# Optimization experiments

Measured on AMD Instinct MI355X. Metric: run time of the kernel, lower is better.

## Reference

```python
import jax, jax.numpy as jnp
import numpy as np

D_MODEL = 2048
N_HEADS = 16
HEAD_DIM = D_MODEL // N_HEADS
THETA = 10000.0


def setup_inputs() -> dict:
    key = jax.random.key(0)
    k1, k2, k3 = jax.random.split(key, 3)
    B, S = 4, 2048
    x = jax.random.normal(k1, (B, S, D_MODEL), dtype=jnp.float32)
    std_qkv = (2.0 / (D_MODEL + 3 * D_MODEL)) ** 0.5
    w_qkv = jax.random.normal(k2, (3 * D_MODEL, D_MODEL), dtype=jnp.float32) * std_qkv
    std_o = (2.0 / (D_MODEL + D_MODEL)) ** 0.5
    w_out = jax.random.normal(k3, (D_MODEL, D_MODEL), dtype=jnp.float32) * std_o
    return {"x": x, "w_qkv": w_qkv, "w_out": w_out}


def _rope(t, cos, sin):
    # t: [H, B, S, hd]; cos/sin: [S, hd/2]; interleaved (even/odd) pairs
    t1 = t[..., 0::2]
    t2 = t[..., 1::2]
    r1 = t1 * cos - t2 * sin
    r2 = t1 * sin + t2 * cos
    return jnp.stack([r1, r2], axis=-1).reshape(t.shape)


def reference(x, w_qkv, w_out):
    B, S, _ = x.shape
    qkv = jnp.einsum('bsd,od->bso', x, w_qkv)  # [B,S,3*D]
    qkv = qkv.reshape(B, S, 3, N_HEADS, HEAD_DIM).transpose(2, 3, 0, 1, 4)  # [3,H,B,S,hd]
    q, k, v = qkv[0], qkv[1], qkv[2]

    pos = jnp.arange(S, dtype=jnp.float32)
    inv_freq = THETA ** (-(jnp.arange(0, HEAD_DIM, 2, dtype=jnp.float32) / HEAD_DIM))
    freqs = pos[:, None] * inv_freq[None, :]  # [S, hd/2]
    cos, sin = jnp.cos(freqs), jnp.sin(freqs)
    q = _rope(q, cos, sin)
    k = _rope(k, cos, sin)

    scores = jnp.einsum('hbqd,hbkd->hbqk', q, k) / jnp.sqrt(jnp.float32(HEAD_DIM))
    causal = jnp.tril(jnp.ones((S, S), dtype=bool))
    scores = jnp.where(causal, scores, -jnp.inf)
    p = jax.nn.softmax(scores, axis=-1)
    a = jnp.einsum('hbqk,hbkd->hbqd', p, v)  # [H,B,S,hd]
    a = a.transpose(1, 2, 0, 3).reshape(B, S, N_HEADS * HEAD_DIM)
    return jnp.einsum('bsd,od->bso', a, w_out)
```

## Files before the change

### kernel.cpp

```cpp
#include <hip/hip_runtime.h>
#include <hip/hip_bf16.h>

typedef __attribute__((ext_vector_type(8))) __bf16 bf16x8;
typedef __attribute__((ext_vector_type(4))) __bf16 bf16x4;
typedef __attribute__((ext_vector_type(4))) float f32x4;
typedef __attribute__((ext_vector_type(4))) unsigned int uintx4;
typedef __attribute__((ext_vector_type(2))) unsigned int uintx2;

__device__ __forceinline__ unsigned short f2bf(float f) {
  __bf16 h = (__bf16)f;
  return __builtin_bit_cast(unsigned short, h);
}
__device__ __forceinline__ float bf2f(unsigned short u) {
  unsigned int x = ((unsigned int)u) << 16;
  return __builtin_bit_cast(float, x);
}
__device__ __forceinline__ bf16x8 ld_frag(const unsigned short* p) {
  return __builtin_bit_cast(bf16x8, *reinterpret_cast<const uintx4*>(p));
}
__device__ __forceinline__ uintx2 cvt4(float4 v) {
  bf16x4 h = { (__bf16)v.x, (__bf16)v.y, (__bf16)v.z, (__bf16)v.w };
  return __builtin_bit_cast(uintx2, h);
}
__device__ __forceinline__ void gload16(const unsigned short* g, unsigned short* l) {
  __builtin_amdgcn_global_load_lds(
      (const __attribute__((address_space(1))) void*)g,
      (__attribute__((address_space(3))) void*)l, 16, 0, 0);
}

__device__ __forceinline__ void cvt8(const float* in, unsigned short* out, int gid) {
  const float4* p = reinterpret_cast<const float4*>(in) + (size_t)gid * 2;
  float4 a = p[0], b = p[1];
  uintx2 lo = cvt4(a), hi = cvt4(b);
  uintx4 o = { lo[0], lo[1], hi[0], hi[1] };
  *(reinterpret_cast<uintx4*>(out) + gid) = o;
}

__global__ __launch_bounds__(256)
void prep(const float* __restrict__ x, unsigned short* __restrict__ xb,
          const float* __restrict__ wqkv, unsigned short* __restrict__ wqkvb,
          float2* __restrict__ tab) {
  const int bid = blockIdx.x, tid = threadIdx.x;
  if (bid < 8192) {
    cvt8(x, xb, bid * 256 + tid);
  } else if (bid < 14336) {
    cvt8(wqkv, wqkvb, (bid - 8192) * 256 + tid);
  } else {
    int gid = (bid - 14336) * 256 + tid;
    int i = gid & 63, s = gid >> 6;
    double inv = pow(10000.0, -(double)i / 64.0);
    double ang = (double)s * inv;
    tab[gid] = make_float2((float)cos(ang), (float)sin(ang));
  }
}

__global__ __launch_bounds__(256)
void cvt_bf16(const float* __restrict__ in, unsigned short* __restrict__ out, int n8) {
  int gid = blockIdx.x * 256 + threadIdx.x;
  if (gid >= n8) return;
  cvt8(in, out, gid);
}

__global__ __launch_bounds__(256)
void rope_kernel(unsigned short* __restrict__ qb, unsigned short* __restrict__ kb,
                 const float2* __restrict__ tab) {
  int gid = blockIdx.x * 256 + threadIdx.x;
  int g = gid & 15;
  int s = (gid >> 4) & 2047;
  int hb = (gid >> 15) & 63;
  unsigned short* base = (gid >> 21) ? kb : qb;
  size_t off = (((size_t)hb * 2048 + s) * 128) + g * 8;
  union { uintx4 u; unsigned short sh[8]; } v;
  v.u = *reinterpret_cast<const uintx4*>(base + off);
  #pragma unroll
  for (int p = 0; p < 4; ++p) {
    float2 cs = tab[s * 64 + g * 4 + p];
    float x1 = bf2f(v.sh[2 * p]), x2 = bf2f(v.sh[2 * p + 1]);
    float r1 = x1 * cs.x - x2 * cs.y;
    float r2 = x1 * cs.y + x2 * cs.x;
    v.sh[2 * p] = f2bf(r1);
    v.sh[2 * p + 1] = f2bf(r2);
  }
  *reinterpret_cast<uintx4*>(base + off) = v.u;
}

template<int EPI>
__global__ __launch_bounds__(512, 1)
void gemm8(const unsigned short* __restrict__ A, const unsigned short* __restrict__ B,
           float* __restrict__ C, unsigned short* __restrict__ qb,
           unsigned short* __restrict__ kb, unsigned short* __restrict__ vtb,
           int M, int N, int K, int nbx) {
  __shared__ unsigned short Al[2][256 * 64];
  __shared__ unsigned short Bl[2][256 * 64];
  const int nwg = gridDim.x, bid = blockIdx.x;
  const int swz = (bid & 7) * (nwg >> 3) + (bid >> 3);
  const int n0 = (swz % nbx) * 256, m0 = (swz / nbx) * 256;
  const int tid = threadIdx.x, lane = tid & 63, w = tid >> 6;
  const int wr = w >> 2, wc = w & 3, l15 = lane & 15, l4 = lane >> 4;
  const int NT = K >> 6;

  auto stage_half = [&](const unsigned short* src, int gr0, unsigned short* ldsb, int kt) {
    #pragma unroll
    for (int i = 0; i < 2; ++i) {
      const int rb = (w * 2 + i) * 8;
      const int R = rb + (lane >> 3);
      const int cs = ((lane & 7) * 8) ^ ((R & 7) << 3);
      gload16(&src[(size_t)(gr0 + R) * K + kt + cs], &ldsb[rb * 64]);
    }
  };
  auto sp_a0b0 = [&](int J) {
    const int buf = J & 1, kt = J * 64;
    stage_half(A, m0, &Al[buf][0], kt);
    stage_half(B, n0, &Bl[buf][0], kt);
  };
  auto sp_b1a1 = [&](int J) {
    const int buf = J & 1, kt = J * 64;
    stage_half(B, n0 + 128, &Bl[buf][128 * 64], kt);
    stage_half(A, m0 + 128, &Al[buf][128 * 64], kt);
  };

  f32x4 acc[8][4];
  const f32x4 z = {0.f, 0.f, 0.f, 0.f};
  #pragma unroll
  for (int mi = 0; mi < 8; ++mi)
    #pragma unroll
    for (int ni = 0; ni < 4; ++ni) acc[mi][ni] = z;

  bf16x8 aF[4][2], bF[4][2];
  auto ldA = [&](int buf, int mh) {
    #pragma unroll
    for (int i = 0; i < 4; ++i) {
      const int R = wr * 128 + (mh * 4 + i) * 16 + l15;
      #pragma unroll
      for (int kk = 0; kk < 2; ++kk)
        aF[i][kk] = ld_frag(&Al[buf][R * 64 + ((kk * 32 + l4 * 8) ^ ((R & 7) << 3))]);
    }
  };
  auto ldB = [&](int buf, int nh) {
    #pragma unroll
    for (int i = 0; i < 2; ++i) {
      const int R = wc * 64 + (nh * 2 + i) * 16 + l15;
      #pragma unroll
      for (int kk = 0; kk < 2; ++kk)
        bF[nh * 2 + i][kk] = ld_frag(&Bl[buf][R * 64 + ((kk * 32 + l4 * 8) ^ ((R & 7) << 3))]);
    }
  };
  auto mm = [&](int mh, int nh) {
    __builtin_amdgcn_s_setprio(1);
    #pragma unroll
    for (int i = 0; i < 4; ++i)
      #pragma unroll
      for (int ii = 0; ii < 2; ++ii)
        #pragma unroll
        for (int kk = 0; kk < 2; ++kk)
          acc[mh * 4 + i][nh * 2 + ii] = __builtin_amdgcn_mfma_f32_16x16x32_bf16(
              aF[i][kk], bF[nh * 2 + ii][kk], acc[mh * 4 + i][nh * 2 + ii], 0, 0, 0);
    __builtin_amdgcn_s_setprio(0);
  };

  sp_a0b0(0); sp_b1a1(0); sp_a0b0(1);
  asm volatile("s_waitcnt vmcnt(4)" ::: "memory");
  __builtin_amdgcn_s_barrier();

  for (int J = 0; J < NT; ++J) {
    const int buf = J & 1;
    ldA(buf, 0);
    ldB(buf, 0);
    if (J + 1 < NT) sp_b1a1(J + 1);
    __builtin_amdgcn_s_barrier();
    asm volatile("s_waitcnt lgkmcnt(0)" ::: "memory");
    mm(0, 0);
    __builtin_amdgcn_s_barrier();
    ldB(buf, 1);
    __builtin_amdgcn_s_barrier();
    asm volatile("s_waitcnt lgkmcnt(0)" ::: "memory");
    mm(0, 1);
    __builtin_amdgcn_s_barrier();
    ldA(buf, 1);
    __builtin_amdgcn_s_barrier();
    asm volatile("s_waitcnt lgkmcnt(0)" ::: "memory");
    mm(1, 0);
    __builtin_amdgcn_s_barrier();
    if (J + 2 < NT) sp_a0b0(J + 2);
    asm volatile("s_waitcnt vmcnt(4)" ::: "memory");
    __builtin_amdgcn_s_barrier();
    mm(1, 1);
    __builtin_amdgcn_s_barrier();
  }

  if constexpr (EPI == 0) {
    #pragma unroll
    for (int mi = 0; mi < 8; ++mi)
      #pragma unroll
      for (int ni = 0; ni < 4; ++ni) {
        const int col = n0 + wc * 64 + ni * 16 + l15;
        #pragma unroll
        for (int j = 0; j < 4; ++j) {
          const int row = m0 + wr * 128 + mi * 16 + l4 * 4 + j;
          C[(size_t)row * N + col] = acc[mi][ni][j];
        }
      }
  } else {
    #pragma unroll
    for (int ni = 0; ni < 4; ++ni) {
      const int col = n0 + wc * 64 + ni * 16 + l15;
      const int t = col >> 11, h = (col >> 7) & 15, d = col & 127;
      #pragma unroll
      for (int mi = 0; mi < 8; ++mi) {
        const int row0 = m0 + wr * 128 + mi * 16 + l4 * 4;
        const int b = row0 >> 11, s0 = row0 & 2047;
        if (t == 2) {
          bf16x4 v4 = { (__bf16)acc[mi][ni][0], (__bf16)acc[mi][ni][1],
                        (__bf16)acc[mi][ni][2], (__bf16)acc[mi][ni][3] };
          *reinterpret_cast<uintx2*>(&vtb[(((size_t)(h * 4 + b)) * 128 + d) * 2048 + s0]) =
              __builtin_bit_cast(uintx2, v4);
        } else {
          unsigned short* base = t ? kb : qb;
          #pragma unroll
          for (int j = 0; j < 4; ++j)
            base[(((size_t)(h * 4 + b)) * 2048 + s0 + j) * 128 + d] = f2bf(acc[mi][ni][j]);
        }
      }
    }
  }
}

__global__ __launch_bounds__(512)
void attn_kernel(const unsigned short* __restrict__ q,
                 const unsigned short* __restrict__ k,
                 const unsigned short* __restrict__ vt,
                 unsigned short* __restrict__ a) {
  const int hb = blockIdx.x;
  const int h = hb >> 2, b = hb & 3;
  const int Q = 15 - blockIdx.y;
  const int q0 = Q * 128;
  const int tid = threadIdx.x, w = tid >> 6, lane = tid & 63;
  const int l15 = lane & 15, l4 = lane >> 4;

  __shared__ unsigned short Klds[64 * 128];
  __shared__ unsigned short Vlds[128 * 64];
  __shared__ unsigned short Plds[8][16 * 64];

  const size_t qkbase = (size_t)hb * 2048 * 128;
  const size_t vtbase = (size_t)hb * 128 * 2048;
  const int qw_min = q0 + w * 16;
  const float scale = 0.08838834764831845f;
  const int nt = 2 * Q + 2;

  bf16x8 qf[4];
  #pragma unroll
  for (int ks = 0; ks < 4; ++ks)
    qf[ks] = ld_frag(&q[qkbase + (size_t)(qw_min + l15) * 128 + ks * 32 + l4 * 8]);

  uintx4 kreg[2], vreg[2];
  auto issue = [&](int kt) {
    #pragma unroll
    for (int i = 0; i < 2; ++i) {
      const int slot = tid + i * 512;
      kreg[i] = *reinterpret_cast<const uintx4*>(
          &k[qkbase + (size_t)(kt + (slot >> 4)) * 128 + (slot & 15) * 8]);
      vreg[i] = *reinterpret_cast<const uintx4*>(
          &vt[vtbase + (size_t)(slot >> 3) * 2048 + kt + (slot & 7) * 8]);
    }
  };
  auto commit = [&]() {
    #pragma unroll
    for (int i = 0; i < 2; ++i) {
      const int slot = tid + i * 512;
      const int kr = slot >> 4, kc = (slot & 15) * 8;
      *reinterpret_cast<uintx4*>(&Klds[kr * 128 + (kc ^ ((kr & 7) << 3))]) = kreg[i];
      const int vr = slot >> 3, vc = (slot & 7) * 8;
      *reinterpret_cast<uintx4*>(&Vlds[vr * 64 + (vc ^ ((vr & 7) << 3))]) = vreg[i];
    }
  };

  float m[4], lsum[4];
  f32x4 acco[8];
  const f32x4 z = {0.f, 0.f, 0.f, 0.f};
  #pragma unroll
  for (int j = 0; j < 4; ++j) { m[j] = -1e30f; lsum[j] = 0.f; }
  #pragma unroll
  for (int d2 = 0; d2 < 8; ++d2) acco[d2] = z;

  issue(0);
  commit();
  __syncthreads();

  for (int t = 0; t < nt; ++t) {
    const int kt = t * 64;
    if (t + 1 < nt) issue(kt + 64);

    f32x4 sc[4];
    #pragma unroll
    for (int c = 0; c < 4; ++c) sc[c] = z;
    __builtin_amdgcn_s_setprio(1);
    #pragma unroll
    for (int c = 0; c < 4; ++c) {
      const int kr = c * 16 + l15;
      #pragma unroll
      for (int ks = 0; ks < 4; ++ks) {
        bf16x8 kf = ld_frag(&Klds[kr * 128 + ((l4 * 8 + ks * 32) ^ ((kr & 7) << 3))]);
        sc[c] = __builtin_amdgcn_mfma_f32_16x16x32_bf16(qf[ks], kf, sc[c], 0, 0, 0);
      }
    }
    __builtin_amdgcn_s_setprio(0);

    #pragma unroll
    for (int c = 0; c < 4; ++c) {
      const int kvg = kt + c * 16 + l15;
      #pragma unroll
      for (int j = 0; j < 4; ++j) {
        const int qg = qw_min + l4 * 4 + j;
        float s = sc[c][j] * scale;
        sc[c][j] = (kvg > qg) ? -1e30f : s;
      }
    }
    float mx[4];
    #pragma unroll
    for (int j = 0; j < 4; ++j)
      mx[j] = fmaxf(fmaxf(sc[0][j], sc[1][j]), fmaxf(sc[2][j], sc[3][j]));
    #pragma unroll
    for (int off = 1; off < 16; off <<= 1)
      #pragma unroll
      for (int j = 0; j < 4; ++j) mx[j] = fmaxf(mx[j], __shfl_xor(mx[j], off));
    bool need = false;
    #pragma unroll
    for (int j = 0; j < 4; ++j) need |= (mx[j] > m[j] + 8.0f);
    if (__any(need)) {
      #pragma unroll
      for (int j = 0; j < 4; ++j) {
        float nm = fmaxf(m[j], mx[j]);
        float al = __expf(m[j] - nm);
        m[j] = nm;
        lsum[j] *= al;
        #pragma unroll
        for (int d2 = 0; d2 < 8; ++d2) acco[d2][j] *= al;
      }
    }
    float rs[4] = {0.f, 0.f, 0.f, 0.f};
    #pragma unroll
    for (int c = 0; c < 4; ++c)
      #pragma unroll
      for (int j = 0; j < 4; ++j) {
        float p = __expf(sc[c][j] - m[j]);
        sc[c][j] = p;
        rs[j] += p;
      }
    #pragma unroll
    for (int off = 1; off < 16; off <<= 1)
      #pragma unroll
      for (int j = 0; j < 4; ++j) rs[j] += __shfl_xor(rs[j], off);
    #pragma unroll
    for (int j = 0; j < 4; ++j) lsum[j] += rs[j];

    #pragma unroll
    for (int c = 0; c < 4; ++c)
      #pragma unroll
      for (int j = 0; j < 4; ++j) {
        const int qr = l4 * 4 + j;
        const int kv = c * 16 + l15;
        Plds[w][qr * 64 + (kv ^ ((qr & 7) << 3))] = f2bf(sc[c][j]);
      }
    __builtin_amdgcn_s_setprio(1);
    #pragma unroll
    for (int g = 0; g < 2; ++g) {
      bf16x8 pf = ld_frag(&Plds[w][l15 * 64 + ((g * 32 + l4 * 8) ^ ((l15 & 7) << 3))]);
      #pragma unroll
      for (int d2 = 0; d2 < 8; ++d2) {
        const int dr = d2 * 16 + l15;
        bf16x8 vf = ld_frag(&Vlds[dr * 64 + ((g * 32 + l4 * 8) ^ ((dr & 7) << 3))]);
        acco[d2] = __builtin_amdgcn_mfma_f32_16x16x32_bf16(pf, vf, acco[d2], 0, 0, 0);
      }
    }
    __builtin_amdgcn_s_setprio(0);

    __syncthreads();
    if (t + 1 < nt) {
      commit();
      __syncthreads();
    }
  }

  #pragma unroll
  for (int j = 0; j < 4; ++j) {
    const float inv = 1.0f / lsum[j];
    const int sr = qw_min + l4 * 4 + j;
    const size_t abase = ((size_t)(b * 2048 + sr)) * 2048 + h * 128;
    #pragma unroll
    for (int d2 = 0; d2 < 8; ++d2)
      a[abase + d2 * 16 + l15] = f2bf(acco[d2][j] * inv);
  }
}

extern "C" void kernel_launch(void* const* d_in, const int* in_sizes, int n_in,
                              void* d_out, int out_size, void* d_ws, size_t ws_size,
                              hipStream_t stream) {
  const float* x = (const float*)d_in[0];
  const float* wqkv = (const float*)d_in[1];
  const float* wout = (const float*)d_in[2];
  float* out = (float*)d_out;
  char* ws = (char*)d_ws;
  char* ob = (char*)d_out;

  unsigned short* qbuf = (unsigned short*)(ws + 0);
  unsigned short* kbuf = (unsigned short*)(ws + 33554432);
  unsigned short* vtb  = (unsigned short*)(ws + 67108864);
  unsigned short* abuf = (unsigned short*)(ws + 100663296);
  unsigned short* woutb = qbuf;
  unsigned short* xb    = (unsigned short*)(ob + 0);
  unsigned short* wqkvb = (unsigned short*)(ob + 33554432);
  float2*         tab   = (float2*)(ob + 58720256);

  hipLaunchKernelGGL(prep, dim3(14848), dim3(256), 0, stream,
                     x, xb, wqkv, wqkvb, tab);
  hipLaunchKernelGGL((gemm8<1>), dim3(768), dim3(512), 0, stream,
                     xb, wqkvb, nullptr, qbuf, kbuf, vtb, 8192, 6144, 2048, 24);
  hipLaunchKernelGGL(rope_kernel, dim3(16384), dim3(256), 0, stream,
                     qbuf, kbuf, (const float2*)tab);
  hipLaunchKernelGGL(attn_kernel, dim3(64, 16), dim3(512), 0, stream,
                     qbuf, kbuf, vtb, abuf);
  hipLaunchKernelGGL(cvt_bf16, dim3(2048), dim3(256), 0, stream, wout, woutb, 524288);
  hipLaunchKernelGGL((gemm8<0>), dim3(256), dim3(512), 0, stream,
                     abuf, woutb, out, nullptr, nullptr, nullptr, 8192, 2048, 2048, 8);
}
```

Before: 497.4 us.

## Fuse RoPE into QKV GEMM epilogue and restructure GEMM LDS pipeline

Removes the standalone RoPE kernel and applies the rotation inside the QKV GEMM epilogue, using a lane shuffle to fetch each pair partner. This drops one full read/write pass over the Q and K buffers. The GEMM main loop is also reorganised: fragments are split into separate A0/A1/B0/B1 registers, and the next tile's first fragments are prefetched before the loop iteration ends. Global staging is regrouped with a deeper initial prefetch. Register pressure rises because of the extra fragment arrays, and the epilogue now does extra table loads.

```diff
diff --git a/kernel.cpp b/kernel.cpp
--- a/kernel.cpp
+++ b/kernel.cpp
@@ -61,35 +61,12 @@
   cvt8(in, out, gid);
 }
 
-__global__ __launch_bounds__(256)
-void rope_kernel(unsigned short* __restrict__ qb, unsigned short* __restrict__ kb,
-                 const float2* __restrict__ tab) {
-  int gid = blockIdx.x * 256 + threadIdx.x;
-  int g = gid & 15;
-  int s = (gid >> 4) & 2047;
-  int hb = (gid >> 15) & 63;
-  unsigned short* base = (gid >> 21) ? kb : qb;
-  size_t off = (((size_t)hb * 2048 + s) * 128) + g * 8;
-  union { uintx4 u; unsigned short sh[8]; } v;
-  v.u = *reinterpret_cast<const uintx4*>(base + off);
-  #pragma unroll
-  for (int p = 0; p < 4; ++p) {
-    float2 cs = tab[s * 64 + g * 4 + p];
-    float x1 = bf2f(v.sh[2 * p]), x2 = bf2f(v.sh[2 * p + 1]);
-    float r1 = x1 * cs.x - x2 * cs.y;
-    float r2 = x1 * cs.y + x2 * cs.x;
-    v.sh[2 * p] = f2bf(r1);
-    v.sh[2 * p + 1] = f2bf(r2);
-  }
-  *reinterpret_cast<uintx4*>(base + off) = v.u;
-}
-
 template<int EPI>
 __global__ __launch_bounds__(512, 1)
 void gemm8(const unsigned short* __restrict__ A, const unsigned short* __restrict__ B,
            float* __restrict__ C, unsigned short* __restrict__ qb,
            unsigned short* __restrict__ kb, unsigned short* __restrict__ vtb,
-           int M, int N, int K, int nbx) {
+           const float2* __restrict__ tab, int M, int N, int K, int nbx) {
   __shared__ unsigned short Al[2][256 * 64];
   __shared__ unsigned short Bl[2][256 * 64];
   const int nwg = gridDim.x, bid = blockIdx.x;
@@ -108,16 +85,10 @@
       gload16(&src[(size_t)(gr0 + R) * K + kt + cs], &ldsb[rb * 64]);
     }
   };
-  auto sp_a0b0 = [&](int J) {
-    const int buf = J & 1, kt = J * 64;
-    stage_half(A, m0, &Al[buf][0], kt);
-    stage_half(B, n0, &Bl[buf][0], kt);
-  };
-  auto sp_b1a1 = [&](int J) {
-    const int buf = J & 1, kt = J * 64;
-    stage_half(B, n0 + 128, &Bl[buf][128 * 64], kt);
-    stage_half(A, m0 + 128, &Al[buf][128 * 64], kt);
-  };
+  auto stA0 = [&](int J) { stage_half(A, m0,       &Al[J & 1][0],        J * 64); };
+  auto stA1 = [&](int J) { stage_half(A, m0 + 128, &Al[J & 1][128 * 64], J * 64); };
+  auto stB0 = [&](int J) { stage_half(B, n0,       &Bl[J & 1][0],        J * 64); };
+  auto stB1 = [&](int J) { stage_half(B, n0 + 128, &Bl[J & 1][128 * 64], J * 64); };
 
   f32x4 acc[8][4];
   const f32x4 z = {0.f, 0.f, 0.f, 0.f};
@@ -126,65 +97,117 @@
     #pragma unroll
     for (int ni = 0; ni < 4; ++ni) acc[mi][ni] = z;
 
-  bf16x8 aF[4][2], bF[4][2];
-  auto ldA = [&](int buf, int mh) {
+  bf16x8 aF0[4][2], aF1[4][2], bF0[2][2], bF1[2][2];
+  auto ldA0 = [&](int buf) {
     #pragma unroll
     for (int i = 0; i < 4; ++i) {
-      const int R = wr * 128 + (mh * 4 + i) * 16 + l15;
+      const int R = wr * 128 + i * 16 + l15;
       #pragma unroll
       for (int kk = 0; kk < 2; ++kk)
-        aF[i][kk] = ld_frag(&Al[buf][R * 64 + ((kk * 32 + l4 * 8) ^ ((R & 7) << 3))]);
-    }
-  };
-  auto ldB = [&](int buf, int nh) {
+        aF0[i][kk] = ld_frag(&Al[buf][R * 64 + ((kk * 32 + l4 * 8) ^ ((R & 7) << 3))]);
+    }
+  };
+  auto ldA1 = [&](int buf) {
+    #pragma unroll
+    for (int i = 0; i < 4; ++i) {
+      const int R = wr * 128 + 64 + i * 16 + l15;
+      #pragma unroll
+      for (int kk = 0; kk < 2; ++kk)
+        aF1[i][kk] = ld_frag(&Al[buf][R * 64 + ((kk * 32 + l4 * 8) ^ ((R & 7) << 3))]);
+    }
+  };
+  auto ldB0 = [&](int buf) {
     #pragma unroll
     for (int i = 0; i < 2; ++i) {
-      const int R = wc * 64 + (nh * 2 + i) * 16 + l15;
+      const int R = wc * 64 + i * 16 + l15;
       #pragma unroll
       for (int kk = 0; kk < 2; ++kk)
-        bF[nh * 2 + i][kk] = ld_frag(&Bl[buf][R * 64 + ((kk * 32 + l4 * 8) ^ ((R & 7) << 3))]);
-    }
-  };
-  auto mm = [&](int mh, int nh) {
-    __builtin_amdgcn_s_setprio(1);
-    #pragma unroll
-    for (int i = 0; i < 4; ++i)
-      #pragma unroll
-      for (int ii = 0; ii < 2; ++ii)
-        #pragma unroll
-        for (int kk = 0; kk < 2; ++kk)
-          acc[mh * 4 + i][nh * 2 + ii] = __builtin_amdgcn_mfma_f32_16x16x32_bf16(
-              aF[i][kk], bF[nh * 2 + ii][kk], acc[mh * 4 + i][nh * 2 + ii], 0, 0, 0);
-    __builtin_amdgcn_s_setprio(0);
-  };
-
-  sp_a0b0(0); sp_b1a1(0); sp_a0b0(1);
-  asm volatile("s_waitcnt vmcnt(4)" ::: "memory");
+        bF0[i][kk] = ld_frag(&Bl[buf][R * 64 + ((kk * 32 + l4 * 8) ^ ((R & 7) << 3))]);
+    }
+  };
+  auto ldB1 = [&](int buf) {
+    #pragma unroll
+    for (int i = 0; i < 2; ++i) {
+      const int R = wc * 64 + 32 + i * 16 + l15;
+      #pragma unroll
+      for (int kk = 0; kk < 2; ++kk)
+        bF1[i][kk] = ld_frag(&Bl[buf][R * 64 + ((kk * 32 + l4 * 8) ^ ((R & 7) << 3))]);
+    }
+  };
+  auto mm00 = [&] {
+    __builtin_amdgcn_s_setprio(1);
+    #pragma unroll
+    for (int kk = 0; kk < 2; ++kk)
+      #pragma unroll
+      for (int i = 0; i < 4; ++i)
+        #pragma unroll
+        for (int ii = 0; ii < 2; ++ii)
+          acc[i][ii] = __builtin_amdgcn_mfma_f32_16x16x32_bf16(aF0[i][kk], bF0[ii][kk], acc[i][ii], 0, 0, 0);
+    __builtin_amdgcn_s_setprio(0);
+  };
+  auto mm01 = [&] {
+    __builtin_amdgcn_s_setprio(1);
+    #pragma unroll
+    for (int kk = 0; kk < 2; ++kk)
+      #pragma unroll
+      for (int i = 0; i < 4; ++i)
+        #pragma unroll
+        for (int ii = 0; ii < 2; ++ii)
+          acc[i][2 + ii] = __builtin_amdgcn_mfma_f32_16x16x32_bf16(aF0[i][kk], bF1[ii][kk], acc[i][2 + ii], 0, 0, 0);
+    __builtin_amdgcn_s_setprio(0);
+  };
+  auto mm10 = [&] {
+    __builtin_amdgcn_s_setprio(1);
+    #pragma unroll
+    for (int kk = 0; kk < 2; ++kk)
+      #pragma unroll
+      for (int i = 0; i < 4; ++i)
+        #pragma unroll
+        for (int ii = 0; ii < 2; ++ii)
+          acc[4 + i][ii] = __builtin_amdgcn_mfma_f32_16x16x32_bf16(aF1[i][kk], bF0[ii][kk], acc[4 + i][ii], 0, 0, 0);
+    __builtin_amdgcn_s_setprio(0);
+  };
+  auto mm11 = [&] {
+    __builtin_amdgcn_s_setprio(1);
+    #pragma unroll
+    for (int kk = 0; kk < 2; ++kk)
+      #pragma unroll
+      for (int i = 0; i < 4; ++i)
+        #pragma unroll
+        for (int ii = 0; ii < 2; ++ii)
+          acc[4 + i][2 + ii] = __builtin_amdgcn_mfma_f32_16x16x32_bf16(aF1[i][kk], bF1[ii][kk], acc[4 + i][2 + ii], 0, 0, 0);
+    __builtin_amdgcn_s_setprio(0);
+  };
+
+  stA0(0); stB0(0); stB1(0); stA1(0);
+  stA0(1); stB0(1); stB1(1); stA1(1);
+  asm volatile("s_waitcnt vmcnt(8)" ::: "memory");
   __builtin_amdgcn_s_barrier();
+  ldA0(0); ldB0(0);
 
   for (int J = 0; J < NT; ++J) {
     const int buf = J & 1;
-    ldA(buf, 0);
-    ldB(buf, 0);
-    if (J + 1 < NT) sp_b1a1(J + 1);
-    __builtin_amdgcn_s_barrier();
-    asm volatile("s_waitcnt lgkmcnt(0)" ::: "memory");
-    mm(0, 0);
-    __builtin_amdgcn_s_barrier();
-    ldB(buf, 1);
-    __builtin_amdgcn_s_barrier();
-    asm volatile("s_waitcnt lgkmcnt(0)" ::: "memory");
-    mm(0, 1);
-    __builtin_amdgcn_s_barrier();
-    ldA(buf, 1);
-    __builtin_amdgcn_s_barrier();
-    asm volatile("s_waitcnt lgkmcnt(0)" ::: "memory");
-    mm(1, 0);
-    __builtin_amdgcn_s_barrier();
-    if (J + 2 < NT) sp_a0b0(J + 2);
-    asm volatile("s_waitcnt vmcnt(4)" ::: "memory");
-    __builtin_amdgcn_s_barrier();
-    mm(1, 1);
+    ldB1(buf);
+    __builtin_amdgcn_s_barrier();
+    mm00();
+    __builtin_amdgcn_s_barrier();
+    ldA1(buf);
+    __builtin_amdgcn_s_barrier();
+    mm01();
+    __builtin_amdgcn_s_barrier();
+    if (J + 2 < NT) { stB0(J + 2); stB1(J + 2); }
+    __builtin_amdgcn_s_barrier();
+    mm10();
+    __builtin_amdgcn_s_barrier();
+    if (J + 2 < NT) {
+      asm volatile("s_waitcnt vmcnt(4)" ::: "memory");
+    } else {
+      asm volatile("s_waitcnt vmcnt(0)" ::: "memory");
+    }
+    if (J + 1 < NT) { ldA0(buf ^ 1); ldB0(buf ^ 1); }
+    if (J + 2 < NT) { stA0(J + 2); stA1(J + 2); }
+    __builtin_amdgcn_s_barrier();
+    mm11();
     __builtin_amdgcn_s_barrier();
   }
 
@@ -217,8 +240,14 @@
         } else {
           unsigned short* base = t ? kb : qb;
           #pragma unroll
-          for (int j = 0; j < 4; ++j)
-            base[(((size_t)(h * 4 + b)) * 2048 + s0 + j) * 128 + d] = f2bf(acc[mi][ni][j]);
+          for (int j = 0; j < 4; ++j) {
+            float v = acc[mi][ni][j];
+            float p = __shfl_xor(v, 1);
+            const int s = s0 + j;
+            float2 cs = tab[s * 64 + (d >> 1)];
+            float r = (d & 1) ? (p * cs.y + v * cs.x) : (v * cs.x - p * cs.y);
+            base[(((size_t)(h * 4 + b)) * 2048 + s) * 128 + d] = f2bf(r);
+          }
         }
       }
     }
@@ -414,12 +443,12 @@
   hipLaunchKernelGGL(prep, dim3(14848), dim3(256), 0, stream,
                      x, xb, wqkv, wqkvb, tab);
   hipLaunchKernelGGL((gemm8<1>), dim3(768), dim3(512), 0, stream,
-                     xb, wqkvb, nullptr, qbuf, kbuf, vtb, 8192, 6144, 2048, 24);
-  hipLaunchKernelGGL(rope_kernel, dim3(16384), dim3(256), 0, stream,
-                     qbuf, kbuf, (const float2*)tab);
+                     xb, wqkvb, nullptr, qbuf, kbuf, vtb, (const float2*)tab,
+                     8192, 6144, 2048, 24);
   hipLaunchKernelGGL(attn_kernel, dim3(64, 16), dim3(512), 0, stream,
                      qbuf, kbuf, vtb, abuf);
   hipLaunchKernelGGL(cvt_bf16, dim3(2048), dim3(256), 0, stream, wout, woutb, 524288);
   hipLaunchKernelGGL((gemm8<0>), dim3(256), dim3(512), 0, stream,
-                     abuf, woutb, out, nullptr, nullptr, nullptr, 8192, 2048, 2048, 8);
-}
+                     abuf, woutb, out, nullptr, nullptr, nullptr, nullptr,
+                     8192, 2048, 2048, 8);
+}
```

Measured after the change: 505.4 us. Within noise of the previous version (+1.6%).

## Transpose attention MFMA layout so softmax is per-lane and P stays in registers

Applied to the files above, without the earlier changes.

Swaps the MFMA operand order so each lane holds one query row's scores. Row max and sum then reduce in-register with only two cross-lane shuffles instead of four-step butterflies on four values. The P tile no longer round-trips through LDS; it is repacked to bf16 and redistributed with lane shuffles into the B-operand layout of the PV MFMA. Output stores become 8-byte vectorized. This removes the LDS writes, reads and scalar P stores at the cost of extra shuffles and selects, and it depends on the fragment lane mapping being right.

```diff
diff --git a/kernel.cpp b/kernel.cpp
--- a/kernel.cpp
+++ b/kernel.cpp
@@ -239,18 +239,18 @@
 
   __shared__ unsigned short Klds[64 * 128];
   __shared__ unsigned short Vlds[128 * 64];
-  __shared__ unsigned short Plds[8][16 * 64];
 
   const size_t qkbase = (size_t)hb * 2048 * 128;
   const size_t vtbase = (size_t)hb * 128 * 2048;
   const int qw_min = q0 + w * 16;
+  const int qg = qw_min + l15;
   const float scale = 0.08838834764831845f;
   const int nt = 2 * Q + 2;
 
   bf16x8 qf[4];
   #pragma unroll
   for (int ks = 0; ks < 4; ++ks)
-    qf[ks] = ld_frag(&q[qkbase + (size_t)(qw_min + l15) * 128 + ks * 32 + l4 * 8]);
+    qf[ks] = ld_frag(&q[qkbase + (size_t)qg * 128 + ks * 32 + l4 * 8]);
 
   uintx4 kreg[2], vreg[2];
   auto issue = [&](int kt) {
@@ -274,13 +274,14 @@
     }
   };
 
-  float m[4], lsum[4];
+  float m = -1e30f, lsum = 0.f;
   f32x4 acco[8];
   const f32x4 z = {0.f, 0.f, 0.f, 0.f};
   #pragma unroll
-  for (int j = 0; j < 4; ++j) { m[j] = -1e30f; lsum[j] = 0.f; }
-  #pragma unroll
   for (int d2 = 0; d2 < 8; ++d2) acco[d2] = z;
+
+  const int srcA = l15 + ((lane & 16) << 1);
+  const bool chi = (lane & 32) != 0;
 
   issue(0);
   commit();
@@ -300,76 +301,78 @@
       #pragma unroll
       for (int ks = 0; ks < 4; ++ks) {
         bf16x8 kf = ld_frag(&Klds[kr * 128 + ((l4 * 8 + ks * 32) ^ ((kr & 7) << 3))]);
-        sc[c] = __builtin_amdgcn_mfma_f32_16x16x32_bf16(qf[ks], kf, sc[c], 0, 0, 0);
+        sc[c] = __builtin_amdgcn_mfma_f32_16x16x32_bf16(kf, qf[ks], sc[c], 0, 0, 0);
       }
     }
     __builtin_amdgcn_s_setprio(0);
 
+    float mx = -1e30f;
     #pragma unroll
     for (int c = 0; c < 4; ++c) {
-      const int kvg = kt + c * 16 + l15;
+      const int kv0 = kt + c * 16 + l4 * 4;
       #pragma unroll
       for (int j = 0; j < 4; ++j) {
-        const int qg = qw_min + l4 * 4 + j;
         float s = sc[c][j] * scale;
-        sc[c][j] = (kvg > qg) ? -1e30f : s;
-      }
-    }
-    float mx[4];
-    #pragma unroll
-    for (int j = 0; j < 4; ++j)
-      mx[j] = fmaxf(fmaxf(sc[0][j], sc[1][j]), fmaxf(sc[2][j], sc[3][j]));
-    #pragma unroll
-    for (int off = 1; off < 16; off <<= 1)
-      #pragma unroll
-      for (int j = 0; j < 4; ++j) mx[j] = fmaxf(mx[j], __shfl_xor(mx[j], off));
-    bool need = false;
-    #pragma unroll
-    for (int j = 0; j < 4; ++j) need |= (mx[j] > m[j] + 8.0f);
-    if (__any(need)) {
+        s = (kv0 + j > qg) ? -1e30f : s;
+        sc[c][j] = s;
+        mx = fmaxf(mx, s);
+      }
+    }
+    mx = fmaxf(mx, __shfl_xor(mx, 16));
+    mx = fmaxf(mx, __shfl_xor(mx, 32));
+    if (__any(mx > m + 8.0f)) {
+      float nm = fmaxf(m, mx);
+      float al = __expf(m - nm);
+      m = nm;
+      lsum *= al;
+      #pragma unroll
+      for (int d2 = 0; d2 < 8; ++d2)
+        #pragma unroll
+        for (int j = 0; j < 4; ++j) acco[d2][j] *= al;
+    }
+    float rs = 0.f;
+    #pragma unroll
+    for (int c = 0; c < 4; ++c)
       #pragma unroll
       for (int j = 0; j < 4; ++j) {
-        float nm = fmaxf(m[j], mx[j]);
-        float al = __expf(m[j] - nm);
-        m[j] = nm;
-        lsum[j] *= al;
-        #pragma unroll
-        for (int d2 = 0; d2 < 8; ++d2) acco[d2][j] *= al;
-      }
-    }
-    float rs[4] = {0.f, 0.f, 0.f, 0.f};
-    #pragma unroll
-    for (int c = 0; c < 4; ++c)
-      #pragma unroll
-      for (int j = 0; j < 4; ++j) {
-        float p = __expf(sc[c][j] - m[j]);
-        sc[c][j] = p;
-        rs[j] += p;
-      }
-    #pragma unroll
-    for (int off = 1; off < 16; off <<= 1)
-      #pragma unroll
-      for (int j = 0; j < 4; ++j) rs[j] += __shfl_xor(rs[j], off);
-    #pragma unroll
-    for (int j = 0; j < 4; ++j) lsum[j] += rs[j];
-
-    #pragma unroll
-    for (int c = 0; c < 4; ++c)
-      #pragma unroll
-      for (int j = 0; j < 4; ++j) {
-        const int qr = l4 * 4 + j;
-        const int kv = c * 16 + l15;
-        Plds[w][qr * 64 + (kv ^ ((qr & 7) << 3))] = f2bf(sc[c][j]);
-      }
+        float pv = __expf(sc[c][j] - m);
+        sc[c][j] = pv;
+        rs += pv;
+      }
+    rs += __shfl_xor(rs, 16);
+    rs += __shfl_xor(rs, 32);
+    lsum += rs;
+
+    unsigned int pk0[4], pk1[4];
+    #pragma unroll
+    for (int c = 0; c < 4; ++c) {
+      pk0[c] = (unsigned)f2bf(sc[c][0]) | ((unsigned)f2bf(sc[c][1]) << 16);
+      pk1[c] = (unsigned)f2bf(sc[c][2]) | ((unsigned)f2bf(sc[c][3]) << 16);
+    }
+
     __builtin_amdgcn_s_setprio(1);
     #pragma unroll
     for (int g = 0; g < 2; ++g) {
-      bf16x8 pf = ld_frag(&Plds[w][l15 * 64 + ((g * 32 + l4 * 8) ^ ((l15 & 7) << 3))]);
+      const int ca = 2 * g, cb = 2 * g + 1;
+      unsigned a0 = (unsigned)__shfl((int)pk0[ca], srcA);
+      unsigned a1 = (unsigned)__shfl((int)pk1[ca], srcA);
+      unsigned b0 = (unsigned)__shfl((int)pk0[cb], srcA);
+      unsigned b1 = (unsigned)__shfl((int)pk1[cb], srcA);
+      unsigned c0 = (unsigned)__shfl((int)pk0[ca], srcA + 16);
+      unsigned c1 = (unsigned)__shfl((int)pk1[ca], srcA + 16);
+      unsigned d0 = (unsigned)__shfl((int)pk0[cb], srcA + 16);
+      unsigned d1 = (unsigned)__shfl((int)pk1[cb], srcA + 16);
+      uintx4 u;
+      u[0] = chi ? b0 : a0;
+      u[1] = chi ? b1 : a1;
+      u[2] = chi ? d0 : c0;
+      u[3] = chi ? d1 : c1;
+      bf16x8 pt = __builtin_bit_cast(bf16x8, u);
       #pragma unroll
       for (int d2 = 0; d2 < 8; ++d2) {
         const int dr = d2 * 16 + l15;
-        bf16x8 vf = ld_frag(&Vlds[dr * 64 + ((g * 32 + l4 * 8) ^ ((dr & 7) << 3))]);
-        acco[d2] = __builtin_amdgcn_mfma_f32_16x16x32_bf16(pf, vf, acco[d2], 0, 0, 0);
+        bf16x8 vf = ld_frag(&Vlds[dr * 64 + ((g * 32 + l4 * 8) ^ ((l15 & 7) << 3))]);
+        acco[d2] = __builtin_amdgcn_mfma_f32_16x16x32_bf16(vf, pt, acco[d2], 0, 0, 0);
       }
     }
     __builtin_amdgcn_s_setprio(0);
@@ -381,14 +384,13 @@
     }
   }
 
+  const float inv = 1.0f / lsum;
+  const size_t abase = ((size_t)(b * 2048 + qg)) * 2048 + h * 128 + l4 * 4;
   #pragma unroll
-  for (int j = 0; j < 4; ++j) {
-    const float inv = 1.0f / lsum[j];
-    const int sr = qw_min + l4 * 4 + j;
-    const size_t abase = ((size_t)(b * 2048 + sr)) * 2048 + h * 128;
-    #pragma unroll
-    for (int d2 = 0; d2 < 8; ++d2)
-      a[abase + d2 * 16 + l15] = f2bf(acco[d2][j] * inv);
+  for (int d2 = 0; d2 < 8; ++d2) {
+    bf16x4 v4 = { (__bf16)(acco[d2][0] * inv), (__bf16)(acco[d2][1] * inv),
+                  (__bf16)(acco[d2][2] * inv), (__bf16)(acco[d2][3] * inv) };
+    *reinterpret_cast<uintx2*>(&a[abase + d2 * 16]) = __builtin_bit_cast(uintx2, v4);
   }
 }
 
@@ -421,5 +423,6 @@
                      qbuf, kbuf, vtb, abuf);
   hipLaunchKernelGGL(cvt_bf16, dim3(2048), dim3(256), 0, stream, wout, woutb, 524288);
   hipLaunchKernelGGL((gemm8<0>), dim3(256), dim3(512), 0, stream,
-                     abuf, woutb, out, nullptr, nullptr, nullptr, 8192, 2048, 2048, 8);
-}
+                     abuf, woutb, out, nullptr, nullptr, nullptr,
+                     8192, 2048, 2048, 8);
+}
```

Result: faster. 479.4 us (-3.6%).
